# Performance work log

Hardware: AMD Instinct MI355X
Metric: run time of the kernel (lower is better)

The kernel has to match this reference:

```python
import jax, jax.numpy as jnp
import numpy as np


def setup_inputs() -> dict:
    key = jax.random.key(0)
    k1, k2 = jax.random.split(key)
    B, C, D = 16384, 4096, 1024
    feat = jax.random.normal(k1, (B, D), dtype=jnp.float32)
    centers = jax.random.normal(k2, (C, D), dtype=jnp.float32)
    return {"feat": feat, "centers": centers}


def reference(feat, centers):
    # Pairwise squared Euclidean distance: dist[b, c] = sum_d (feat[b,d] - centers[c,d])^2
    # materializing the O(B*C*D) broadcast difference (same math as the torch module).
    x2 = jnp.sum(feat * feat, axis=-1, keepdims=True)          # [B, 1]
    c2 = jnp.sum(centers * centers, axis=-1)[None, :]          # [1, C]
    xc = jnp.einsum("bd,cd->bc", feat, centers)                # [B, C] GEMM
    dist = x2 + c2 - 2.0 * xc
    return dist
```

## Files before the change

kernel.cpp:

```cpp
#include <hip/hip_runtime.h>
#include <hip/hip_bf16.h>

typedef __bf16 bf16x8 __attribute__((ext_vector_type(8)));
typedef float floatx4 __attribute__((ext_vector_type(4)));

__device__ __forceinline__ unsigned f2bf(float f) {
    unsigned u = __float_as_uint(f);
    u += 0x7FFFu + ((u >> 16) & 1u);
    return u >> 16;
}

__device__ __forceinline__ void gl2lds(const void* g, void* l) {
    void* gnc = const_cast<void*>(g);
    __builtin_amdgcn_global_load_lds(
        (__attribute__((address_space(1))) void*)gnc,
        (__attribute__((address_space(3))) void*)l,
        16, 0, 0);
}

__global__ __launch_bounds__(256) void cast_norm2(
    const float* __restrict__ feat, const float* __restrict__ cent,
    unsigned short* __restrict__ Ab, unsigned short* __restrict__ Bb,
    float* __restrict__ x2, float* __restrict__ c2, int M)
{
    const int tid  = threadIdx.x;
    const int half = tid >> 7;
    const int t    = tid & 127;
    const int row  = blockIdx.x * 2 + half;

    const float* src;
    unsigned short* dst;
    float* nrm;
    if (row < M) {
        src = feat + (size_t)row * 1024;
        dst = Ab   + (size_t)row * 1024;
        nrm = x2 + row;
    } else {
        const int r = row - M;
        src = cent + (size_t)r * 1024;
        dst = Bb   + (size_t)r * 1024;
        nrm = c2 + r;
    }

    const float4 v0 = ((const float4*)src)[t * 2];
    const float4 v1 = ((const float4*)src)[t * 2 + 1];
    float s = v0.x * v0.x + v0.y * v0.y + v0.z * v0.z + v0.w * v0.w
            + v1.x * v1.x + v1.y * v1.y + v1.z * v1.z + v1.w * v1.w;

    uint4 o;
    o.x = f2bf(v0.x) | (f2bf(v0.y) << 16);
    o.y = f2bf(v0.z) | (f2bf(v0.w) << 16);
    o.z = f2bf(v1.x) | (f2bf(v1.y) << 16);
    o.w = f2bf(v1.z) | (f2bf(v1.w) << 16);
    ((uint4*)dst)[t] = o;

#pragma unroll
    for (int off = 32; off > 0; off >>= 1) s += __shfl_down(s, off);
    __shared__ float ws[4];
    if ((tid & 63) == 0) ws[tid >> 6] = s;
    __syncthreads();
    if (t == 0) *nrm = ws[half * 2] + ws[half * 2 + 1];
}

__global__ __launch_bounds__(256) void dist_gemm(
    const unsigned short* __restrict__ A,
    const unsigned short* __restrict__ B,
    const float* __restrict__ x2,
    const float* __restrict__ c2,
    float* __restrict__ out,
    int M, int N)
{
    constexpr int K = 1024;
    __shared__ unsigned short sA[128 * 32];
    __shared__ unsigned short sB[128 * 32];

    const int tid  = threadIdx.x;
    const int wave = tid >> 6;
    const int lane = tid & 63;
    const int quad = lane >> 4;
    const int l16  = lane & 15;
    const int wm   = wave & 1;
    const int wn   = wave >> 1;

    const int gx  = gridDim.x;
    const int lin = blockIdx.y * gx + blockIdx.x;
    const int colsPerXcd = gx >> 3;
    const int xcd  = lin & 7;
    const int slot = lin >> 3;
    const int bx = xcd * colsPerXcd + (slot % colsPerXcd);
    const int by = slot / colsPerXcd;

    const int blockRow = by * 128;
    const int blockCol = bx * 128;

    const int srow = lane >> 2;
    const int scol = (lane & 3) * 8;

    unsigned short* ldsA0 = sA + wave * 512;
    unsigned short* ldsA1 = sA + (wave + 4) * 512;
    unsigned short* ldsB0 = sB + wave * 512;
    unsigned short* ldsB1 = sB + (wave + 4) * 512;

    const unsigned short* gA0 = A + (size_t)(blockRow + wave * 16 + srow) * K + scol;
    const unsigned short* gA1 = A + (size_t)(blockRow + (wave + 4) * 16 + srow) * K + scol;
    const unsigned short* gB0 = B + (size_t)(blockCol + wave * 16 + srow) * K + scol;
    const unsigned short* gB1 = B + (size_t)(blockCol + (wave + 4) * 16 + srow) * K + scol;

    floatx4 acc[4][4];
#pragma unroll
    for (int i = 0; i < 4; i++)
#pragma unroll
        for (int j = 0; j < 4; j++) acc[i][j] = (floatx4){0.f, 0.f, 0.f, 0.f};

    const bf16x8* fragA[4];
    const bf16x8* fragB[4];
#pragma unroll
    for (int i = 0; i < 4; i++) {
        fragA[i] = (const bf16x8*)(sA + ((wm * 64 + i * 16 + l16) * 32 + quad * 8));
        fragB[i] = (const bf16x8*)(sB + ((wn * 64 + i * 16 + l16) * 32 + quad * 8));
    }

    for (int k0 = 0; k0 < K; k0 += 32) {
        __syncthreads();
        gl2lds(gA0 + k0, ldsA0);
        gl2lds(gA1 + k0, ldsA1);
        gl2lds(gB0 + k0, ldsB0);
        gl2lds(gB1 + k0, ldsB1);
        __syncthreads();

        bf16x8 a[4], b[4];
#pragma unroll
        for (int i = 0; i < 4; i++) a[i] = *fragA[i];
#pragma unroll
        for (int j = 0; j < 4; j++) b[j] = *fragB[j];
#pragma unroll
        for (int i = 0; i < 4; i++)
#pragma unroll
            for (int j = 0; j < 4; j++)
                acc[i][j] = __builtin_amdgcn_mfma_f32_16x16x32_bf16(a[i], b[j], acc[i][j], 0, 0, 0);
    }

    float c2v[4];
#pragma unroll
    for (int j = 0; j < 4; j++) c2v[j] = c2[blockCol + wn * 64 + j * 16 + l16];

#pragma unroll
    for (int i = 0; i < 4; i++) {
        const int rowb = blockRow + wm * 64 + i * 16 + quad * 4;
        float x2v[4];
#pragma unroll
        for (int r = 0; r < 4; r++) x2v[r] = x2[rowb + r];
#pragma unroll
        for (int j = 0; j < 4; j++) {
            const int col = blockCol + wn * 64 + j * 16 + l16;
            float* o = out + (size_t)rowb * N + col;
#pragma unroll
            for (int r = 0; r < 4; r++)
                o[(size_t)r * N] = fmaf(-2.0f, acc[i][j][r], x2v[r] + c2v[j]);
        }
    }
}

__global__ __launch_bounds__(256) void dist_fallback(
    const float* __restrict__ A, const float* __restrict__ B,
    float* __restrict__ out, int M, int N, int K)
{
    __shared__ float sA[64][17];
    __shared__ float sB[64][17];
    const int tid = threadIdx.x;
    const int tx = tid & 15;
    const int ty = tid >> 4;
    const int rowBase = blockIdx.y * 64;
    const int colBase = blockIdx.x * 64;
    float acc[4][4] = {};
    for (int k0 = 0; k0 < K; k0 += 16) {
        __syncthreads();
        {
            const int r = tid >> 2, c = (tid & 3) * 4;
            float4 va = *(const float4*)(A + (size_t)(rowBase + r) * K + k0 + c);
            sA[r][c] = va.x; sA[r][c + 1] = va.y; sA[r][c + 2] = va.z; sA[r][c + 3] = va.w;
            float4 vb = *(const float4*)(B + (size_t)(colBase + r) * K + k0 + c);
            sB[r][c] = vb.x; sB[r][c + 1] = vb.y; sB[r][c + 2] = vb.z; sB[r][c + 3] = vb.w;
        }
        __syncthreads();
#pragma unroll
        for (int kk = 0; kk < 16; kk++) {
            float ra[4], rb[4];
#pragma unroll
            for (int i = 0; i < 4; i++) ra[i] = sA[ty * 4 + i][kk];
#pragma unroll
            for (int j = 0; j < 4; j++) rb[j] = sB[tx * 4 + j][kk];
#pragma unroll
            for (int i = 0; i < 4; i++)
#pragma unroll
                for (int j = 0; j < 4; j++) {
                    float d = ra[i] - rb[j];
                    acc[i][j] = fmaf(d, d, acc[i][j]);
                }
        }
    }
#pragma unroll
    for (int i = 0; i < 4; i++)
#pragma unroll
        for (int j = 0; j < 4; j++)
            out[(size_t)(rowBase + ty * 4 + i) * N + (colBase + tx * 4 + j)] = acc[i][j];
}

extern "C" void kernel_launch(void* const* d_in, const int* in_sizes, int n_in,
                              void* d_out, int out_size, void* d_ws, size_t ws_size,
                              hipStream_t stream) {
    const float* feat = (const float*)d_in[0];
    const float* cent = (const float*)d_in[1];
    float* out = (float*)d_out;

    const int D = 1024;
    const int M = in_sizes[0] / D;
    const int N = in_sizes[1] / D;

    const size_t offA  = 0;
    const size_t offB  = offA + (size_t)M * D * sizeof(unsigned short);
    const size_t offX2 = offB + (size_t)N * D * sizeof(unsigned short);
    const size_t offC2 = offX2 + (size_t)M * sizeof(float);
    const size_t need  = offC2 + (size_t)N * sizeof(float);

    if (ws_size >= need && (M % 1024) == 0 && (N % 1024) == 0) {
        unsigned short* Ab = (unsigned short*)((char*)d_ws + offA);
        unsigned short* Bb = (unsigned short*)((char*)d_ws + offB);
        float* x2 = (float*)((char*)d_ws + offX2);
        float* c2 = (float*)((char*)d_ws + offC2);

        cast_norm2<<<(M + N) / 2, 256, 0, stream>>>(feat, cent, Ab, Bb, x2, c2, M);
        dist_gemm<<<dim3(N / 128, M / 128), 256, 0, stream>>>(Ab, Bb, x2, c2, out, M, N);
    } else {
        dist_fallback<<<dim3(N / 64, M / 64), 256, 0, stream>>>(feat, cent, out, M, N, D);
    }
}
```

Baseline: 470.1 us.

## Rewrite distance GEMM as 256x256 tile, 8-wave double-buffered LDS pipeline

Replaces the 128x128, single-buffered bf16 MFMA kernel with a 256x256 tile computed by 512 threads. K steps are 64 wide, LDS is double-buffered (128 KB) with XOR-swizzled layout, and global-to-LDS loads are interleaved with MFMA groups using explicit barriers, vmcnt waits and s_setprio. The goal is to hide global load latency, raise arithmetic intensity per tile and reduce LDS bank conflicts. In exchange it uses far more LDS and registers per block and hard-codes K=1024, and the fast path now requires N to be a multiple of 2048.

```diff
diff --git a/kernel.cpp b/kernel.cpp
--- a/kernel.cpp
+++ b/kernel.cpp
@@ -62,7 +62,7 @@
     if (t == 0) *nrm = ws[half * 2] + ws[half * 2 + 1];
 }
 
-__global__ __launch_bounds__(256) void dist_gemm(
+__global__ __launch_bounds__(512, 2) void dist_gemm(
     const unsigned short* __restrict__ A,
     const unsigned short* __restrict__ B,
     const float* __restrict__ x2,
@@ -70,17 +70,17 @@
     float* __restrict__ out,
     int M, int N)
 {
-    constexpr int K = 1024;
-    __shared__ unsigned short sA[128 * 32];
-    __shared__ unsigned short sB[128 * 32];
+    __shared__ alignas(16) char lds_raw[131072];
+    char* ldsb = lds_raw;
+    const char* ldsc = lds_raw;
 
     const int tid  = threadIdx.x;
     const int wave = tid >> 6;
     const int lane = tid & 63;
     const int quad = lane >> 4;
     const int l16  = lane & 15;
-    const int wm   = wave & 1;
-    const int wn   = wave >> 1;
+    const int wm   = wave >> 2;
+    const int wn   = wave & 3;
 
     const int gx  = gridDim.x;
     const int lin = blockIdx.y * gx + blockIdx.x;
@@ -90,75 +90,149 @@
     const int bx = xcd * colsPerXcd + (slot % colsPerXcd);
     const int by = slot / colsPerXcd;
 
-    const int blockRow = by * 128;
-    const int blockCol = bx * 128;
-
-    const int srow = lane >> 2;
-    const int scol = (lane & 3) * 8;
-
-    unsigned short* ldsA0 = sA + wave * 512;
-    unsigned short* ldsA1 = sA + (wave + 4) * 512;
-    unsigned short* ldsB0 = sB + wave * 512;
-    unsigned short* ldsB1 = sB + (wave + 4) * 512;
-
-    const unsigned short* gA0 = A + (size_t)(blockRow + wave * 16 + srow) * K + scol;
-    const unsigned short* gA1 = A + (size_t)(blockRow + (wave + 4) * 16 + srow) * K + scol;
-    const unsigned short* gB0 = B + (size_t)(blockCol + wave * 16 + srow) * K + scol;
-    const unsigned short* gB1 = B + (size_t)(blockCol + (wave + 4) * 16 + srow) * K + scol;
-
-    floatx4 acc[4][4];
-#pragma unroll
-    for (int i = 0; i < 4; i++)
-#pragma unroll
-        for (int j = 0; j < 4; j++) acc[i][j] = (floatx4){0.f, 0.f, 0.f, 0.f};
-
-    const bf16x8* fragA[4];
-    const bf16x8* fragB[4];
-#pragma unroll
-    for (int i = 0; i < 4; i++) {
-        fragA[i] = (const bf16x8*)(sA + ((wm * 64 + i * 16 + l16) * 32 + quad * 8));
-        fragB[i] = (const bf16x8*)(sB + ((wn * 64 + i * 16 + l16) * 32 + quad * 8));
-    }
-
-    for (int k0 = 0; k0 < K; k0 += 32) {
-        __syncthreads();
-        gl2lds(gA0 + k0, ldsA0);
-        gl2lds(gA1 + k0, ldsA1);
-        gl2lds(gB0 + k0, ldsB0);
-        gl2lds(gB1 + k0, ldsB1);
-        __syncthreads();
-
-        bf16x8 a[4], b[4];
-#pragma unroll
-        for (int i = 0; i < 4; i++) a[i] = *fragA[i];
-#pragma unroll
-        for (int j = 0; j < 4; j++) b[j] = *fragB[j];
-#pragma unroll
-        for (int i = 0; i < 4; i++)
-#pragma unroll
-            for (int j = 0; j < 4; j++)
-                acc[i][j] = __builtin_amdgcn_mfma_f32_16x16x32_bf16(a[i], b[j], acc[i][j], 0, 0, 0);
-    }
+    const int blockRow = by * 256;
+    const int blockCol = bx * 256;
+
+    const int cswz = (lane & 3) ^ (((lane >> 5) & 1) << 1);
+    const unsigned short* pA = A + (size_t)(blockRow + wave * 16 + (lane >> 2)) * 1024 + cswz * 8;
+    const unsigned short* pB = B + (size_t)(blockCol + wave * 16 + (lane >> 2)) * 1024 + cswz * 8;
+    const int stOff = wave * 1024;
+
+#define STAGE_A(buf, kt, h) do {                                              \
+        const unsigned short* _s = pA + (size_t)(h) * 131072 + (kt) * 64;     \
+        char* _d = ldsb + (buf) * 65536 + (h) * 8192 + stOff;                 \
+        gl2lds(_s,      _d);                                                  \
+        gl2lds(_s + 32, _d + 16384);                                          \
+    } while (0)
+#define STAGE_B(buf, kt, h) do {                                              \
+        const unsigned short* _s = pB + (size_t)(h) * 131072 + (kt) * 64;     \
+        char* _d = ldsb + (buf) * 65536 + 32768 + (h) * 8192 + stOff;         \
+        gl2lds(_s,      _d);                                                  \
+        gl2lds(_s + 32, _d + 16384);                                          \
+    } while (0)
+
+    const int swq = quad ^ ((l16 & 8) >> 2);
+    const int aRd = (wm * 128 + l16) * 64 + swq * 16;
+    const int bRd = 32768 + (wn * 64 + l16) * 64 + swq * 16;
+
+#define RD_A(buf, ks, mf) (*(const bf16x8*)(ldsc + (buf) * 65536 + (ks) * 16384 + (mf) * 1024 + aRd))
+#define RD_B(buf, ks, nf) (*(const bf16x8*)(ldsc + (buf) * 65536 + (ks) * 16384 + (nf) * 1024 + bRd))
+
+#define LOAD_A8(arr, buf, ks) do {                                            \
+        arr[0] = RD_A(buf, ks, 0); arr[1] = RD_A(buf, ks, 1);                 \
+        arr[2] = RD_A(buf, ks, 2); arr[3] = RD_A(buf, ks, 3);                 \
+        arr[4] = RD_A(buf, ks, 4); arr[5] = RD_A(buf, ks, 5);                 \
+        arr[6] = RD_A(buf, ks, 6); arr[7] = RD_A(buf, ks, 7);                 \
+    } while (0)
+#define LOAD_B4(arr, buf, ks) do {                                            \
+        arr[0] = RD_B(buf, ks, 0); arr[1] = RD_B(buf, ks, 1);                 \
+        arr[2] = RD_B(buf, ks, 2); arr[3] = RD_B(buf, ks, 3);                 \
+    } while (0)
+
+#define BAR()    do { __builtin_amdgcn_s_barrier(); asm volatile("" ::: "memory"); } while (0)
+#define LGKM0()  asm volatile("s_waitcnt lgkmcnt(0)" ::: "memory")
+#define VMCNT4() asm volatile("s_waitcnt vmcnt(4)" ::: "memory")
+#define VMCNT0() asm volatile("s_waitcnt vmcnt(0)" ::: "memory")
+
+#define MFMA16(aa, mo, bb) do {                                               \
+        __builtin_amdgcn_s_setprio(1);                                        \
+        _Pragma("unroll")                                                     \
+        for (int _m = 0; _m < 4; ++_m) {                                      \
+            _Pragma("unroll")                                                 \
+            for (int _n = 0; _n < 4; ++_n) {                                  \
+                acc[(mo) + _m][_n] = __builtin_amdgcn_mfma_f32_16x16x32_bf16( \
+                    aa[(mo) + _m], bb[_n], acc[(mo) + _m][_n], 0, 0, 0);      \
+            }                                                                 \
+        }                                                                     \
+        __builtin_amdgcn_s_setprio(0);                                        \
+    } while (0)
+
+    floatx4 acc[8][4];
+#pragma unroll
+    for (int i = 0; i < 8; ++i)
+#pragma unroll
+        for (int j = 0; j < 4; ++j) acc[i][j] = (floatx4){0.f, 0.f, 0.f, 0.f};
+
+    bf16x8 a0[8], a1[8], b0[4], b1[4];
+
+    STAGE_A(0, 0, 0); STAGE_A(0, 0, 1);
+    STAGE_B(0, 0, 0); STAGE_B(0, 0, 1);
+    STAGE_A(1, 1, 0); STAGE_A(1, 1, 1);
+    VMCNT4();
+    BAR();
+
+#define K_ITER(T, S) do {                                                     \
+                                                                      \
+        LOAD_A8(a0, 0, 0); LOAD_B4(b0, 0, 0);                                 \
+        STAGE_B(1, (T) + 1, 0);                                               \
+        BAR(); LGKM0(); MFMA16(a0, 0, b0); BAR();                             \
+                                                                      \
+        LOAD_A8(a1, 0, 1); LOAD_B4(b1, 0, 1);                                 \
+        STAGE_B(1, (T) + 1, 1);                                               \
+        BAR(); LGKM0(); MFMA16(a0, 4, b0); BAR();                             \
+                                                                      \
+        if (S) STAGE_A(0, (T) + 2, 0);                                        \
+        BAR(); MFMA16(a1, 0, b1); BAR();                                      \
+                                                                      \
+        if (S) STAGE_A(0, (T) + 2, 1);                                        \
+        BAR(); MFMA16(a1, 4, b1);                                             \
+        if (S) { VMCNT4(); } else { VMCNT0(); }                               \
+        BAR();                                                                \
+                                                                      \
+        LOAD_A8(a0, 1, 0); LOAD_B4(b0, 1, 0);                                 \
+        if (S) STAGE_B(0, (T) + 2, 0);                                        \
+        BAR(); LGKM0(); MFMA16(a0, 0, b0); BAR();                             \
+                                                                      \
+        LOAD_A8(a1, 1, 1); LOAD_B4(b1, 1, 1);                                 \
+        if (S) STAGE_B(0, (T) + 2, 1);                                        \
+        BAR(); LGKM0(); MFMA16(a0, 4, b0); BAR();                             \
+                                                                      \
+        if (S) STAGE_A(1, (T) + 3, 0);                                        \
+        BAR(); MFMA16(a1, 0, b1); BAR();                                      \
+                                                                      \
+        if (S) STAGE_A(1, (T) + 3, 1);                                        \
+        BAR(); MFMA16(a1, 4, b1); VMCNT4(); BAR();                            \
+    } while (0)
+
+#pragma unroll 1
+    for (int it = 0; it < 7; ++it) {
+        const int T = it * 2;
+        K_ITER(T, true);
+    }
+    K_ITER(14, false);
 
     float c2v[4];
 #pragma unroll
-    for (int j = 0; j < 4; j++) c2v[j] = c2[blockCol + wn * 64 + j * 16 + l16];
-
-#pragma unroll
-    for (int i = 0; i < 4; i++) {
-        const int rowb = blockRow + wm * 64 + i * 16 + quad * 4;
+    for (int nf = 0; nf < 4; ++nf) c2v[nf] = c2[blockCol + wn * 64 + nf * 16 + l16];
+
+#pragma unroll
+    for (int mf = 0; mf < 8; ++mf) {
+        const int rowb = blockRow + wm * 128 + mf * 16 + quad * 4;
         float x2v[4];
 #pragma unroll
-        for (int r = 0; r < 4; r++) x2v[r] = x2[rowb + r];
-#pragma unroll
-        for (int j = 0; j < 4; j++) {
-            const int col = blockCol + wn * 64 + j * 16 + l16;
+        for (int r = 0; r < 4; ++r) x2v[r] = x2[rowb + r];
+#pragma unroll
+        for (int nf = 0; nf < 4; ++nf) {
+            const int col = blockCol + wn * 64 + nf * 16 + l16;
             float* o = out + (size_t)rowb * N + col;
 #pragma unroll
-            for (int r = 0; r < 4; r++)
-                o[(size_t)r * N] = fmaf(-2.0f, acc[i][j][r], x2v[r] + c2v[j]);
+            for (int r = 0; r < 4; ++r)
+                o[(size_t)r * N] = fmaf(-2.0f, acc[mf][nf][r], x2v[r] + c2v[nf]);
         }
     }
+
+#undef K_ITER
+#undef MFMA16
+#undef VMCNT0
+#undef VMCNT4
+#undef LGKM0
+#undef BAR
+#undef LOAD_B4
+#undef LOAD_A8
+#undef RD_B
+#undef RD_A
+#undef STAGE_B
+#undef STAGE_A
 }
 
 __global__ __launch_bounds__(256) void dist_fallback(
@@ -223,14 +297,14 @@
     const size_t offC2 = offX2 + (size_t)M * sizeof(float);
     const size_t need  = offC2 + (size_t)N * sizeof(float);
 
-    if (ws_size >= need && (M % 1024) == 0 && (N % 1024) == 0) {
+    if (ws_size >= need && (M % 256) == 0 && (N % 2048) == 0) {
         unsigned short* Ab = (unsigned short*)((char*)d_ws + offA);
         unsigned short* Bb = (unsigned short*)((char*)d_ws + offB);
         float* x2 = (float*)((char*)d_ws + offX2);
         float* c2 = (float*)((char*)d_ws + offC2);
 
         cast_norm2<<<(M + N) / 2, 256, 0, stream>>>(feat, cent, Ab, Bb, x2, c2, M);
-        dist_gemm<<<dim3(N / 128, M / 128), 256, 0, stream>>>(Ab, Bb, x2, c2, out, M, N);
+        dist_gemm<<<dim3(N / 256, M / 256), 512, 0, stream>>>(Ab, Bb, x2, c2, out, M, N);
     } else {
         dist_fallback<<<dim3(N / 64, M / 64), 256, 0, stream>>>(feat, cent, out, M, N, D);
     }
```

Result: faster. 430.8 us (-8.4%).
